# Kernel tuning notes

Measured on AMD Instinct MI355X. Metric: run time of the kernel, lower is better.

## Reference

```python
import jax, jax.numpy as jnp
import numpy as np

K = 16            # neighbors
QUERY_CHUNK = 256 # SE is applied per chunk of this many query points (matches torch loop)
EPS = 1e-5        # BatchNorm eps (eval mode, running stats)


def bn(x, g, b, m, v):
    # eval-mode batchnorm over last axis (channel-last layout here)
    return (x - m) * (g / jnp.sqrt(v + EPS)) + b


def setup_inputs() -> dict:
    key = jax.random.key(0)
    ks = jax.random.split(key, 16)
    B, Cin, N = 4, 128, 4096
    H, Cout = 128, 256
    se_h = Cout // 4
    r = lambda k, s, sc=1.0: jax.random.normal(k, s, jnp.float32) * sc
    return dict(
        x=r(ks[0], (B, Cin, N)),
        W_edge=r(ks[1], (H, 2 * Cin), 0.05),          # edge_mlp conv2d 1x1
        bn1_g=jnp.ones((H,), jnp.float32), bn1_b=jnp.zeros((H,), jnp.float32),
        bn1_m=r(ks[2], (H,), 0.1), bn1_v=jax.random.uniform(ks[3], (H,), jnp.float32) + 0.5,
        w_att=r(ks[4], (H,), 0.1),                     # att_conv (1,H,1,1)
        W_fuse=r(ks[5], (Cout, H), 0.05),              # fuse conv1d
        bn2_g=jnp.ones((Cout,), jnp.float32), bn2_b=jnp.zeros((Cout,), jnp.float32),
        bn2_m=r(ks[6], (Cout,), 0.1), bn2_v=jax.random.uniform(ks[7], (Cout,), jnp.float32) + 0.5,
        fc1_w=r(ks[8], (se_h, Cout), 0.05), fc1_b=jnp.zeros((se_h,), jnp.float32),
        fc2_w=r(ks[9], (Cout, se_h), 0.05), fc2_b=jnp.zeros((Cout,), jnp.float32),
        W_res=r(ks[10], (Cout, Cin), 0.05),            # res_conv conv1d (in!=out)
        bn3_g=jnp.ones((Cout,), jnp.float32), bn3_b=jnp.zeros((Cout,), jnp.float32),
        bn3_m=r(ks[11], (Cout,), 0.1), bn3_v=jax.random.uniform(ks[12], (Cout,), jnp.float32) + 0.5,
    )


def reference(x, W_edge, bn1_g, bn1_b, bn1_m, bn1_v, w_att,
              W_fuse, bn2_g, bn2_b, bn2_m, bn2_v,
              fc1_w, fc1_b, fc2_w, fc2_b,
              W_res, bn3_g, bn3_b, bn3_m, bn3_v):
    B, Cin, N = x.shape
    x_t = jnp.swapaxes(x, 1, 2)  # (B,N,Cin)

    # KNN on features (dynamic=False -> knn on x.transpose); squared euclidean
    # has the same ordering as torch.cdist(p=2).
    sq = jnp.sum(x_t * x_t, axis=-1)                               # (B,N)
    d2 = sq[:, :, None] + sq[:, None, :] - 2.0 * jnp.einsum('bnc,bmc->bnm', x_t, x_t)
    _, idx = jax.lax.top_k(-d2, K)                                  # (B,N,K) smallest dists

    neigh = jax.vmap(lambda p, i: p[i])(x_t, idx)                   # (B,N,K,Cin)
    center = jnp.broadcast_to(x_t[:, :, None, :], neigh.shape)      # (B,N,K,Cin)
    edge = jnp.concatenate([neigh - center, center], axis=-1)       # (B,N,K,2Cin)

    # edge_mlp: 1x1 conv + BN + ReLU
    h = jax.nn.relu(bn(jnp.einsum('bnkc,hc->bnkh', edge, W_edge),
                       bn1_g, bn1_b, bn1_m, bn1_v))                 # (B,N,K,H)

    # attention over neighbors
    att = jax.nn.softmax(jnp.einsum('bnkh,h->bnk', h, w_att), axis=-1)
    agg = jnp.einsum('bnkh,bnk->bnh', h, att)                       # (B,N,H)

    # fuse conv1d + BN + ReLU
    out = jax.nn.relu(bn(jnp.einsum('bnh,oh->bno', agg, W_fuse),
                         bn2_g, bn2_b, bn2_m, bn2_v))               # (B,N,Cout)

    # SE channel attention, applied per query chunk (matches torch loop semantics)
    Cout = out.shape[-1]
    nc = N // QUERY_CHUNK
    oc = out.reshape(B, nc, QUERY_CHUNK, Cout)
    s = oc.mean(axis=2)                                             # (B,nc,Cout)
    s = jax.nn.relu(jnp.einsum('bmc,hc->bmh', s, fc1_w) + fc1_b)
    s = jax.nn.sigmoid(jnp.einsum('bmh,ch->bmc', s, fc2_w) + fc2_b)
    out = (oc * s[:, :, None, :]).reshape(B, N, Cout)

    # residual projection (in_channels != out_channels)
    res = bn(jnp.einsum('bnc,oc->bno', x_t, W_res), bn3_g, bn3_b, bn3_m, bn3_v)
    out = out + res
    return jnp.swapaxes(out, 1, 2)                                  # (B,Cout,N)
```

## Files before the change

kernel.cpp:

```cpp
#include <hip/hip_runtime.h>
#include <cstddef>

typedef __bf16 bf16;
typedef __bf16 bf16x8 __attribute__((ext_vector_type(8)));
typedef float  f32x4  __attribute__((ext_vector_type(4)));
typedef unsigned short u16;
typedef unsigned long long u64;

#define MFMA16x16(a, b, c) __builtin_amdgcn_mfma_f32_16x16x32_bf16((a), (b), (c), 0, 0, 0)

namespace {
constexpr int BB   = 4;
constexpr int CIN  = 128;
constexpr int NPT  = 4096;
constexpr int KNBR = 16;
constexpr int HED  = 128;
constexpr int COUT = 256;
}

__device__ __forceinline__ unsigned int ord_f32(float f) {
  unsigned int b = __float_as_uint(f);
  return b ^ (0x80000000u | (unsigned int)((int)b >> 31));
}
__device__ __forceinline__ u64 mk_key(float d, int m) {
  return ((u64)ord_f32(d) << 32) | (unsigned int)m;
}

__device__ __forceinline__ void sort16(u64* k) {
  #pragma unroll
  for (int sz = 2; sz <= 16; sz <<= 1) {
    #pragma unroll
    for (int st = sz >> 1; st > 0; st >>= 1) {
      #pragma unroll
      for (int i = 0; i < 16; ++i) {
        const int j = i ^ st;
        if (j > i) {
          const bool up = ((i & sz) == 0);
          const u64 a = k[i], c = k[j];
          const bool sw = up ? (a > c) : (a < c);
          k[i] = sw ? c : a;
          k[j] = sw ? a : c;
        }
      }
    }
  }
}

__device__ __forceinline__ void merge16(u64* R, const u64* B) {
  u64 t[16];
  #pragma unroll
  for (int i = 0; i < 16; ++i) {
    const u64 a = R[i], c = B[15 - i];
    t[i] = (a < c) ? a : c;
  }
  #pragma unroll
  for (int st = 8; st > 0; st >>= 1) {
    #pragma unroll
    for (int i = 0; i < 16; ++i) {
      const int j = i ^ st;
      if (j > i) {
        const u64 a = t[i], c = t[j];
        const bool sw = a > c;
        t[i] = sw ? c : a;
        t[j] = sw ? a : c;
      }
    }
  }
  #pragma unroll
  for (int i = 0; i < 16; ++i) R[i] = t[i];
}

__global__ __launch_bounds__(256) void k_wconv(const float* __restrict__ We,
                                               const float* __restrict__ Wf,
                                               const float* __restrict__ Wr,
                                               bf16* __restrict__ Web,
                                               bf16* __restrict__ Wfb,
                                               bf16* __restrict__ Wrb) {
  const int i = blockIdx.x * 256 + threadIdx.x;
  const int a = i >> 15;
  const int j = i & 32767;
  const float* src = (a == 0) ? We : (a == 1) ? Wf : Wr;
  bf16*        dst = (a == 0) ? Web : (a == 1) ? Wfb : Wrb;
  dst[j] = (bf16)src[j];
}

__global__ __launch_bounds__(256) void k_prep(const float* __restrict__ x,
                                              bf16* __restrict__ xh,
                                              bf16* __restrict__ xl,
                                              float* __restrict__ sq) {
  __shared__ __attribute__((aligned(16))) bf16 th[64][136];
  __shared__ __attribute__((aligned(16))) bf16 tl[64][136];
  __shared__ float sqp[4][64];
  const int tid = threadIdx.x;
  const int b   = blockIdx.x >> 6;
  const int n0  = (blockIdx.x & 63) << 6;
  const int nl  = tid & 63;
  const int cg  = tid >> 6;
  const float* xb = x + (size_t)b * CIN * NPT;
  float acc = 0.f;
  #pragma unroll
  for (int rep = 0; rep < 32; ++rep) {
    const int c = rep * 4 + cg;
    const float v = xb[(size_t)c * NPT + n0 + nl];
    const bf16 h = (bf16)v;
    const bf16 l = (bf16)(v - (float)h);
    acc += v * v;
    th[nl][c] = h;
    tl[nl][c] = l;
  }
  sqp[cg][nl] = acc;
  __syncthreads();
  bf16* xho = xh + ((size_t)b * NPT + n0) * CIN;
  bf16* xlo = xl + ((size_t)b * NPT + n0) * CIN;
  #pragma unroll
  for (int rep = 0; rep < 32; ++rep) {
    const int e = rep * 256 + tid;
    const int r = e >> 7;
    const int c = e & 127;
    xho[(size_t)r * CIN + c] = th[r][c];
    xlo[(size_t)r * CIN + c] = tl[r][c];
  }
  if (tid < 64) {
    sq[b * NPT + n0 + tid] = sqp[0][tid] + sqp[1][tid] + sqp[2][tid] + sqp[3][tid];
  }
}

__global__ __launch_bounds__(256, 2) void k_knn(const bf16* __restrict__ xh,
                                                const bf16* __restrict__ xl,
                                                const float* __restrict__ sq,
                                                int* __restrict__ knn_idx) {
  __shared__ u64 Lk[32][258];
  const int tid  = threadIdx.x;
  const int w    = tid >> 6;
  const int lane = tid & 63;
  const int col  = lane & 15;
  const int quad = lane >> 4;
  const int b    = blockIdx.x >> 7;
  const int q0   = (blockIdx.x & 127) << 5;
  const bf16*  xhb = xh + (size_t)b * NPT * CIN;
  const bf16*  xlb = xl + (size_t)b * NPT * CIN;
  const float* sqb = sq + b * NPT;

  bf16x8 qh[2][4], ql[2][4];
  float sqn[2];
  #pragma unroll
  for (int t = 0; t < 2; ++t) {
    const bf16* qrh = xhb + (size_t)(q0 + t * 16 + col) * CIN + quad * 8;
    const bf16* qrl = xlb + (size_t)(q0 + t * 16 + col) * CIN + quad * 8;
    #pragma unroll
    for (int ks = 0; ks < 4; ++ks) {
      qh[t][ks] = *(const bf16x8*)(qrh + ks * 32);
      ql[t][ks] = *(const bf16x8*)(qrl + ks * 32);
    }
    sqn[t] = sqb[q0 + t * 16 + col];
  }

  u64 R0[16], R1[16];
  #pragma unroll
  for (int i = 0; i < 16; ++i) { R0[i] = ~0ull; R1[i] = ~0ull; }

  const int cbase = w << 10;
  for (int mt = 0; mt < 16; ++mt) {
    const int m0 = cbase + (mt << 6);
    u64 k0[16], k1[16];
    #pragma unroll
    for (int cb = 0; cb < 4; ++cb) {
      const bf16* crh = xhb + (size_t)(m0 + cb * 16 + col) * CIN + quad * 8;
      const bf16* crl = xlb + (size_t)(m0 + cb * 16 + col) * CIN + quad * 8;
      f32x4 a0 = {0.f, 0.f, 0.f, 0.f};
      f32x4 a1 = {0.f, 0.f, 0.f, 0.f};
      #pragma unroll
      for (int ks = 0; ks < 4; ++ks) {
        const bf16x8 ch_ = *(const bf16x8*)(crh + ks * 32);
        const bf16x8 cl_ = *(const bf16x8*)(crl + ks * 32);
        a0 = MFMA16x16(cl_, qh[0][ks], a0);
        a0 = MFMA16x16(ch_, ql[0][ks], a0);
        a0 = MFMA16x16(ch_, qh[0][ks], a0);
        a1 = MFMA16x16(cl_, qh[1][ks], a1);
        a1 = MFMA16x16(ch_, ql[1][ks], a1);
        a1 = MFMA16x16(ch_, qh[1][ks], a1);
      }
      const f32x4 sqm = *(const f32x4*)(sqb + m0 + cb * 16 + quad * 4);
      #pragma unroll
      for (int r = 0; r < 4; ++r) {
        const int m = m0 + cb * 16 + quad * 4 + r;
        k0[cb * 4 + r] = mk_key((sqn[0] + sqm[r]) - 2.0f * a0[r], m);
        k1[cb * 4 + r] = mk_key((sqn[1] + sqm[r]) - 2.0f * a1[r], m);
      }
    }
    sort16(k0); merge16(R0, k0);
    sort16(k1); merge16(R1, k1);
  }

  {
    const int run = (w << 2) | quad;
    const int qA = col;
    const int qB = 16 | col;
    #pragma unroll
    for (int i = 0; i < 16; ++i) {
      Lk[qA][run * 16 + i] = R0[i];
      Lk[qB][run * 16 + i] = R1[i];
    }
  }
  __syncthreads();

  #pragma unroll
  for (int half = 8; half >= 1; half >>= 1) {
    u64 A[16], Bv[16];
    const bool act = tid < 32 * half;
    const int q = tid / half;
    const int j = tid % half;
    if (act) {
      #pragma unroll
      for (int i = 0; i < 16; ++i) {
        A[i]  = Lk[q][(2 * j) * 16 + i];
        Bv[i] = Lk[q][(2 * j + 1) * 16 + i];
      }
    }
    __syncthreads();
    if (act) {
      merge16(A, Bv);
      #pragma unroll
      for (int i = 0; i < 16; ++i) Lk[q][j * 16 + i] = A[i];
    }
    __syncthreads();
  }

  if (tid < 32) {
    int* op = knn_idx + (size_t)(b * NPT + q0 + tid) * KNBR;
    #pragma unroll
    for (int i = 0; i < 16; ++i) op[i] = (int)(Lk[tid][i] & 0xFFFFFFFFull);
  }
}

__global__ __launch_bounds__(256) void k_edge(const bf16* __restrict__ xh,
                                              const bf16* __restrict__ xl,
                                              const int* __restrict__ knn_idx,
                                              const bf16* __restrict__ We,
                                              const float* __restrict__ g1, const float* __restrict__ b1,
                                              const float* __restrict__ m1, const float* __restrict__ v1,
                                              const float* __restrict__ watt,
                                              bf16* __restrict__ agg) {
  __shared__ __attribute__((aligned(16))) bf16 Ew[4][16][264];
  __shared__ float s1[HED], t1[HED], wat[HED];
  const int tid  = threadIdx.x;
  const int w    = tid >> 6;
  const int lane = tid & 63;
  const int col  = lane & 15;
  const int quad = lane >> 4;
  if (tid < HED) {
    const float ss = g1[tid] / sqrtf(v1[tid] + 1e-5f);
    s1[tid] = ss;
    t1[tid] = b1[tid] - m1[tid] * ss;
    wat[tid] = watt[tid];
  }
  __syncthreads();
  const int gw = blockIdx.x * 4 + w;
  for (int it = 0; it < 4; ++it) {
    const int p = gw * 4 + it;
    const int b = p >> 12;
    const int n = p & 4095;
    const bf16* xhb = xh + (size_t)b * NPT * CIN;
    const bf16* xlb = xl + (size_t)b * NPT * CIN;
    const int my = knn_idx[(size_t)p * KNBR + col];
    const int m  = __shfl(my, lane >> 2);
    const int sub = lane & 3;
    const int kn  = lane >> 2;
    const bf16* nh = xhb + (size_t)m * CIN + sub * 32;
    const bf16* nl_ = xlb + (size_t)m * CIN + sub * 32;
    const bf16* ch = xhb + (size_t)n * CIN + sub * 32;
    const bf16* cl = xlb + (size_t)n * CIN + sub * 32;
    #pragma unroll
    for (int j = 0; j < 4; ++j) {
      const bf16x8 nhv = *(const bf16x8*)(nh + j * 8);
      const bf16x8 nlv = *(const bf16x8*)(nl_ + j * 8);
      const bf16x8 chv = *(const bf16x8*)(ch + j * 8);
      const bf16x8 clv = *(const bf16x8*)(cl + j * 8);
      bf16x8 dv, cv;
      #pragma unroll
      for (int e = 0; e < 8; ++e) {
        const float nf = (float)nhv[e] + (float)nlv[e];
        const float cf = (float)chv[e] + (float)clv[e];
        dv[e] = (bf16)(nf - cf);
        cv[e] = (bf16)cf;
      }
      *(bf16x8*)&Ew[w][kn][sub * 32 + j * 8]       = dv;
      *(bf16x8*)&Ew[w][kn][128 + sub * 32 + j * 8] = cv;
    }
    __syncthreads();
    const f32x4 zero4 = {0.f, 0.f, 0.f, 0.f};
    f32x4 acc[8];
    #pragma unroll
    for (int hb = 0; hb < 8; ++hb) acc[hb] = zero4;
    #pragma unroll
    for (int ks = 0; ks < 8; ++ks) {
      const bf16x8 af = *(const bf16x8*)&Ew[w][col][ks * 32 + quad * 8];
      #pragma unroll
      for (int hb = 0; hb < 8; ++hb) {
        const bf16x8 bfv = *(const bf16x8*)(We + (size_t)(hb * 16 + col) * 256 + ks * 32 + quad * 8);
        acc[hb] = MFMA16x16(af, bfv, acc[hb]);
      }
    }
    float h[8][4];
    float lg[4] = {0.f, 0.f, 0.f, 0.f};
    #pragma unroll
    for (int hb = 0; hb < 8; ++hb) {
      const int hc = hb * 16 + col;
      const float ss = s1[hc], tt = t1[hc], ww = wat[hc];
      #pragma unroll
      for (int r = 0; r < 4; ++r) {
        const float hv = fmaxf(acc[hb][r] * ss + tt, 0.f);
        h[hb][r] = hv;
        lg[r] += hv * ww;
      }
    }
    #pragma unroll
    for (int r = 0; r < 4; ++r) {
      float vv = lg[r];
      vv += __shfl_xor(vv, 1);
      vv += __shfl_xor(vv, 2);
      vv += __shfl_xor(vv, 4);
      vv += __shfl_xor(vv, 8);
      lg[r] = vv;
    }
    float mx = fmaxf(fmaxf(lg[0], lg[1]), fmaxf(lg[2], lg[3]));
    mx = fmaxf(mx, __shfl_xor(mx, 16));
    mx = fmaxf(mx, __shfl_xor(mx, 32));
    float ex[4];
    float sm = 0.f;
    #pragma unroll
    for (int r = 0; r < 4; ++r) { ex[r] = expf(lg[r] - mx); sm += ex[r]; }
    sm += __shfl_xor(sm, 16);
    sm += __shfl_xor(sm, 32);
    const float inv = 1.0f / sm;
    float ag[8];
    #pragma unroll
    for (int hb = 0; hb < 8; ++hb) {
      float a = h[hb][0] * ex[0] + h[hb][1] * ex[1] + h[hb][2] * ex[2] + h[hb][3] * ex[3];
      a += __shfl_xor(a, 16);
      a += __shfl_xor(a, 32);
      ag[hb] = a * inv;
    }
    if (quad == 0) {
      bf16* ao = agg + (size_t)p * HED;
      #pragma unroll
      for (int hb = 0; hb < 8; ++hb) ao[hb * 16 + col] = (bf16)ag[hb];
    }
    __syncthreads();
  }
}

__global__ __launch_bounds__(256) void k_fuse(const bf16* __restrict__ agg,
                                              const bf16* __restrict__ Wf,
                                              const float* __restrict__ g2, const float* __restrict__ b2,
                                              const float* __restrict__ m2, const float* __restrict__ v2,
                                              bf16* __restrict__ outp) {
  const int tid  = threadIdx.x;
  const int w    = tid >> 6;
  const int lane = tid & 63;
  const int col  = lane & 15;
  const int quad = lane >> 4;
  const int p0   = (blockIdx.x * 4 + w) * 16;
  bf16x8 afr[4];
  const bf16* arow = agg + (size_t)(p0 + col) * HED + quad * 8;
  #pragma unroll
  for (int ks = 0; ks < 4; ++ks) afr[ks] = *(const bf16x8*)(arow + ks * 32);
  #pragma unroll
  for (int ob = 0; ob < 16; ++ob) {
    f32x4 acc = {0.f, 0.f, 0.f, 0.f};
    const bf16* brow = Wf + (size_t)(ob * 16 + col) * HED + quad * 8;
    #pragma unroll
    for (int ks = 0; ks < 4; ++ks)
      acc = MFMA16x16(afr[ks], *(const bf16x8*)(brow + ks * 32), acc);
    const int o = ob * 16 + col;
    const float ss = g2[o] / sqrtf(v2[o] + 1e-5f);
    const float tt = b2[o] - m2[o] * ss;
    #pragma unroll
    for (int r = 0; r < 4; ++r) {
      outp[(size_t)(p0 + quad * 4 + r) * COUT + o] = (bf16)fmaxf(acc[r] * ss + tt, 0.f);
    }
  }
}

__global__ __launch_bounds__(256) void k_se(const bf16* __restrict__ outp,
                                            const float* __restrict__ f1w, const float* __restrict__ f1b,
                                            const float* __restrict__ f2w, const float* __restrict__ f2b,
                                            float* __restrict__ sse) {
  __shared__ float mean_s[COUT];
  __shared__ float h1[64];
  const int bc  = blockIdx.x;
  const int tid = threadIdx.x;
  const bf16* base = outp + (size_t)bc * 256 * COUT;
  float s = 0.f;
  for (int p2 = 0; p2 < 256; ++p2) s += (float)base[(size_t)p2 * COUT + tid];
  mean_s[tid] = s * (1.0f / 256.0f);
  __syncthreads();
  if (tid < 64) {
    float a = f1b[tid];
    for (int c = 0; c < COUT; ++c) a += f1w[tid * COUT + c] * mean_s[c];
    h1[tid] = fmaxf(a, 0.f);
  }
  __syncthreads();
  float a = f2b[tid];
  #pragma unroll
  for (int j = 0; j < 64; ++j) a += f2w[tid * 64 + j] * h1[j];
  sse[(size_t)bc * COUT + tid] = 1.0f / (1.0f + expf(-a));
}

__global__ __launch_bounds__(256) void k_final(const bf16* __restrict__ xh,
                                               const bf16* __restrict__ Wr,
                                               const float* __restrict__ g3, const float* __restrict__ b3,
                                               const float* __restrict__ m3, const float* __restrict__ v3,
                                               const bf16* __restrict__ outp,
                                               const float* __restrict__ sse,
                                               float* __restrict__ out) {
  const int tid  = threadIdx.x;
  const int w    = tid >> 6;
  const int lane = tid & 63;
  const int col  = lane & 15;
  const int quad = lane >> 4;
  const int p0   = (blockIdx.x * 4 + w) * 16;
  const int b    = p0 >> 12;
  const int n0l  = p0 & 4095;
  bf16x8 afr[4];
  const bf16* arow = xh + (size_t)(p0 + col) * CIN + quad * 8;
  #pragma unroll
  for (int ks = 0; ks < 4; ++ks) afr[ks] = *(const bf16x8*)(arow + ks * 32);
  const float* scb = sse + (size_t)(b * 16 + (n0l >> 8)) * COUT;
  #pragma unroll
  for (int ob = 0; ob < 16; ++ob) {
    f32x4 acc = {0.f, 0.f, 0.f, 0.f};
    const bf16* brow = Wr + (size_t)(ob * 16 + col) * CIN + quad * 8;
    #pragma unroll
    for (int ks = 0; ks < 4; ++ks)
      acc = MFMA16x16(afr[ks], *(const bf16x8*)(brow + ks * 32), acc);
    const int o = ob * 16 + col;
    const float ss = g3[o] / sqrtf(v3[o] + 1e-5f);
    const float tt = b3[o] - m3[o] * ss;
    const float sc = scb[o];
    f32x4 pk;
    #pragma unroll
    for (int r = 0; r < 4; ++r) {
      const float res = acc[r] * ss + tt;
      pk[r] = (float)outp[(size_t)(p0 + quad * 4 + r) * COUT + o] * sc + res;
    }
    float* op = out + (size_t)(b * COUT + o) * NPT + n0l + quad * 4;
    *(f32x4*)op = pk;
  }
}

extern "C" void kernel_launch(void* const* d_in, const int* in_sizes, int n_in,
                              void* d_out, int out_size, void* d_ws, size_t ws_size,
                              hipStream_t stream) {
  (void)in_sizes; (void)n_in; (void)out_size; (void)ws_size;
  const float* x    = (const float*)d_in[0];
  const float* We   = (const float*)d_in[1];
  const float* g1   = (const float*)d_in[2];
  const float* b1   = (const float*)d_in[3];
  const float* m1   = (const float*)d_in[4];
  const float* v1   = (const float*)d_in[5];
  const float* watt = (const float*)d_in[6];
  const float* Wf   = (const float*)d_in[7];
  const float* g2   = (const float*)d_in[8];
  const float* b2   = (const float*)d_in[9];
  const float* m2   = (const float*)d_in[10];
  const float* v2   = (const float*)d_in[11];
  const float* f1w  = (const float*)d_in[12];
  const float* f1b  = (const float*)d_in[13];
  const float* f2w  = (const float*)d_in[14];
  const float* f2b  = (const float*)d_in[15];
  const float* Wr   = (const float*)d_in[16];
  const float* g3   = (const float*)d_in[17];
  const float* b3   = (const float*)d_in[18];
  const float* m3   = (const float*)d_in[19];
  const float* v3   = (const float*)d_in[20];

  char* ws = (char*)d_ws;
  size_t off = 0;
  bf16*  xth  = (bf16*)(ws + off);  off += (size_t)BB * NPT * CIN * 2;
  bf16*  xtl  = (bf16*)(ws + off);  off += (size_t)BB * NPT * CIN * 2;
  float* sq   = (float*)(ws + off); off += (size_t)BB * NPT * 4;
  int*   idxp = (int*)(ws + off);   off += (size_t)BB * NPT * KNBR * 4;
  bf16*  aggp = (bf16*)(ws + off);  off += (size_t)BB * NPT * HED * 2;
  bf16*  outp = (bf16*)(ws + off);  off += (size_t)BB * NPT * COUT * 2;
  float* ssep = (float*)(ws + off); off += (size_t)BB * 16 * COUT * 4;
  bf16*  Web  = (bf16*)(ws + off);  off += (size_t)HED * 2 * CIN * 2;
  bf16*  Wfb  = (bf16*)(ws + off);  off += (size_t)COUT * HED * 2;
  bf16*  Wrb  = (bf16*)(ws + off);  off += (size_t)COUT * CIN * 2;

  float* out = (float*)d_out;

  k_wconv<<<384, 256, 0, stream>>>(We, Wf, Wr, Web, Wfb, Wrb);
  k_prep<<<256, 256, 0, stream>>>(x, xth, xtl, sq);
  k_knn<<<512, 256, 0, stream>>>(xth, xtl, sq, idxp);
  k_edge<<<1024, 256, 0, stream>>>(xth, xtl, idxp, Web, g1, b1, m1, v1, watt, aggp);
  k_fuse<<<256, 256, 0, stream>>>(aggp, Wfb, g2, b2, m2, v2, outp);
  k_se<<<64, 256, 0, stream>>>(outp, f1w, f1b, f2w, f2b, ssep);
  k_final<<<256, 256, 0, stream>>>(xth, Wrb, g3, b3, m3, v3, outp, ssep, out);
}
```

Before: 427.4 us.

## Halve KNN queries per block and merge partial top-k lists via wave shuffles

```diff
diff --git a/kernel.cpp b/kernel.cpp
--- a/kernel.cpp
+++ b/kernel.cpp
@@ -68,6 +68,13 @@
   }
   #pragma unroll
   for (int i = 0; i < 16; ++i) R[i] = t[i];
+}
+
+__device__ __forceinline__ void shfl_merge16(u64* R, int mask) {
+  u64 B[16];
+  #pragma unroll
+  for (int i = 0; i < 16; ++i) B[i] = __shfl_xor(R[i], mask, 64);
+  merge16(R, B);
 }
 
 __global__ __launch_bounds__(256) void k_wconv(const float* __restrict__ We,
@@ -125,111 +132,100 @@
   }
 }
 
-__global__ __launch_bounds__(256, 2) void k_knn(const bf16* __restrict__ xh,
+__global__ __launch_bounds__(256, 4) void k_knn(const bf16* __restrict__ xh,
                                                 const bf16* __restrict__ xl,
                                                 const float* __restrict__ sq,
                                                 int* __restrict__ knn_idx) {
-  __shared__ u64 Lk[32][258];
+  __shared__ u64 Lk[16][66];
   const int tid  = threadIdx.x;
   const int w    = tid >> 6;
   const int lane = tid & 63;
   const int col  = lane & 15;
   const int quad = lane >> 4;
-  const int b    = blockIdx.x >> 7;
-  const int q0   = (blockIdx.x & 127) << 5;
+  const int b    = blockIdx.x >> 8;
+  const int q0   = (blockIdx.x & 255) << 4;
   const bf16*  xhb = xh + (size_t)b * NPT * CIN;
   const bf16*  xlb = xl + (size_t)b * NPT * CIN;
   const float* sqb = sq + b * NPT;
 
-  bf16x8 qh[2][4], ql[2][4];
-  float sqn[2];
-  #pragma unroll
-  for (int t = 0; t < 2; ++t) {
-    const bf16* qrh = xhb + (size_t)(q0 + t * 16 + col) * CIN + quad * 8;
-    const bf16* qrl = xlb + (size_t)(q0 + t * 16 + col) * CIN + quad * 8;
+  bf16x8 qh[4], ql[4];
+  {
+    const bf16* qrh = xhb + (size_t)(q0 + col) * CIN + quad * 8;
+    const bf16* qrl = xlb + (size_t)(q0 + col) * CIN + quad * 8;
     #pragma unroll
     for (int ks = 0; ks < 4; ++ks) {
-      qh[t][ks] = *(const bf16x8*)(qrh + ks * 32);
-      ql[t][ks] = *(const bf16x8*)(qrl + ks * 32);
-    }
-    sqn[t] = sqb[q0 + t * 16 + col];
-  }
-
-  u64 R0[16], R1[16];
-  #pragma unroll
-  for (int i = 0; i < 16; ++i) { R0[i] = ~0ull; R1[i] = ~0ull; }
+      qh[ks] = *(const bf16x8*)(qrh + ks * 32);
+      ql[ks] = *(const bf16x8*)(qrl + ks * 32);
+    }
+  }
+  const float sqn = sqb[q0 + col];
+
+  u64 R[16];
+  #pragma unroll
+  for (int i = 0; i < 16; ++i) R[i] = ~0ull;
 
   const int cbase = w << 10;
   for (int mt = 0; mt < 16; ++mt) {
     const int m0 = cbase + (mt << 6);
-    u64 k0[16], k1[16];
+    u64 k[16];
     #pragma unroll
     for (int cb = 0; cb < 4; ++cb) {
       const bf16* crh = xhb + (size_t)(m0 + cb * 16 + col) * CIN + quad * 8;
       const bf16* crl = xlb + (size_t)(m0 + cb * 16 + col) * CIN + quad * 8;
       f32x4 a0 = {0.f, 0.f, 0.f, 0.f};
-      f32x4 a1 = {0.f, 0.f, 0.f, 0.f};
       #pragma unroll
       for (int ks = 0; ks < 4; ++ks) {
         const bf16x8 ch_ = *(const bf16x8*)(crh + ks * 32);
         const bf16x8 cl_ = *(const bf16x8*)(crl + ks * 32);
-        a0 = MFMA16x16(cl_, qh[0][ks], a0);
-        a0 = MFMA16x16(ch_, ql[0][ks], a0);
-        a0 = MFMA16x16(ch_, qh[0][ks], a0);
-        a1 = MFMA16x16(cl_, qh[1][ks], a1);
-        a1 = MFMA16x16(ch_, ql[1][ks], a1);
-        a1 = MFMA16x16(ch_, qh[1][ks], a1);
+        a0 = MFMA16x16(cl_, qh[ks], a0);
+        a0 = MFMA16x16(ch_, ql[ks], a0);
+        a0 = MFMA16x16(ch_, qh[ks], a0);
       }
       const f32x4 sqm = *(const f32x4*)(sqb + m0 + cb * 16 + quad * 4);
       #pragma unroll
       for (int r = 0; r < 4; ++r) {
         const int m = m0 + cb * 16 + quad * 4 + r;
-        k0[cb * 4 + r] = mk_key((sqn[0] + sqm[r]) - 2.0f * a0[r], m);
-        k1[cb * 4 + r] = mk_key((sqn[1] + sqm[r]) - 2.0f * a1[r], m);
-      }
-    }
-    sort16(k0); merge16(R0, k0);
-    sort16(k1); merge16(R1, k1);
-  }
-
-  {
-    const int run = (w << 2) | quad;
-    const int qA = col;
-    const int qB = 16 | col;
+        k[cb * 4 + r] = mk_key((sqn + sqm[r]) - 2.0f * a0[r], m);
+      }
+    }
+    sort16(k);
+    merge16(R, k);
+  }
+
+  shfl_merge16(R, 16);
+  shfl_merge16(R, 32);
+
+  if (quad == 0) {
+    #pragma unroll
+    for (int i = 0; i < 16; ++i) Lk[col][w * 16 + i] = R[i];
+  }
+  __syncthreads();
+
+  if (tid < 32) {
+    const int q = tid >> 1;
+    const int j = tid & 1;
+    u64 A[16], Bv[16];
     #pragma unroll
     for (int i = 0; i < 16; ++i) {
-      Lk[qA][run * 16 + i] = R0[i];
-      Lk[qB][run * 16 + i] = R1[i];
-    }
-  }
-  __syncthreads();
-
-  #pragma unroll
-  for (int half = 8; half >= 1; half >>= 1) {
+      A[i]  = Lk[q][(2 * j) * 16 + i];
+      Bv[i] = Lk[q][(2 * j + 1) * 16 + i];
+    }
+    merge16(A, Bv);
+    #pragma unroll
+    for (int i = 0; i < 16; ++i) Lk[q][j * 16 + i] = A[i];
+  }
+  __syncthreads();
+  if (tid < 16) {
     u64 A[16], Bv[16];
-    const bool act = tid < 32 * half;
-    const int q = tid / half;
-    const int j = tid % half;
-    if (act) {
-      #pragma unroll
-      for (int i = 0; i < 16; ++i) {
-        A[i]  = Lk[q][(2 * j) * 16 + i];
-        Bv[i] = Lk[q][(2 * j + 1) * 16 + i];
-      }
-    }
-    __syncthreads();
-    if (act) {
-      merge16(A, Bv);
-      #pragma unroll
-      for (int i = 0; i < 16; ++i) Lk[q][j * 16 + i] = A[i];
-    }
-    __syncthreads();
-  }
-
-  if (tid < 32) {
+    #pragma unroll
+    for (int i = 0; i < 16; ++i) {
+      A[i]  = Lk[tid][i];
+      Bv[i] = Lk[tid][16 + i];
+    }
+    merge16(A, Bv);
     int* op = knn_idx + (size_t)(b * NPT + q0 + tid) * KNBR;
     #pragma unroll
-    for (int i = 0; i < 16; ++i) op[i] = (int)(Lk[tid][i] & 0xFFFFFFFFull);
+    for (int i = 0; i < 16; ++i) op[i] = (int)(A[i] & 0xFFFFFFFFull);
   }
 }
 
@@ -492,7 +488,7 @@
 
   k_wconv<<<384, 256, 0, stream>>>(We, Wf, Wr, Web, Wfb, Wrb);
   k_prep<<<256, 256, 0, stream>>>(x, xth, xtl, sq);
-  k_knn<<<512, 256, 0, stream>>>(xth, xtl, sq, idxp);
+  k_knn<<<1024, 256, 0, stream>>>(xth, xtl, sq, idxp);
   k_edge<<<1024, 256, 0, stream>>>(xth, xtl, idxp, Web, g1, b1, m1, v1, watt, aggp);
   k_fuse<<<256, 256, 0, stream>>>(aggp, Wfb, g2, b2, m2, v2, outp);
   k_se<<<64, 256, 0, stream>>>(outp, f1w, f1b, f2w, f2b, ssep);
```

Result: slower. 557.2 us (+30.4%).
